# Kernel tuning notes

Measured on AMD Instinct MI355X. Metric: run time of the kernel, lower is better.

Reference implementation:

```python
import jax, jax.numpy as jnp
import numpy as np

B, T, C = 4, 4096, 1024   # batch, seq_len, n_embd
HS = 128                  # tamanho_cabeca (head size)


def setup_inputs() -> dict:
    key = jax.random.key(0)
    kx, kq, kk, kv = jax.random.split(key, 4)
    scale = 0.02
    return {
        "x": jax.random.normal(kx, (B, T, C), dtype=jnp.float32),
        "Wq": jax.random.normal(kq, (C, HS), dtype=jnp.float32) * scale,
        "Wk": jax.random.normal(kk, (C, HS), dtype=jnp.float32) * scale,
        "Wv": jax.random.normal(kv, (C, HS), dtype=jnp.float32) * scale,
    }


def reference(x, Wq, Wk, Wv):
    # Single-head causal self-attention, faithful to the torch Head module.
    _, Tn, Cn = x.shape
    q = jnp.einsum("btc,ch->bth", x, Wq)
    k = jnp.einsum("btc,ch->bth", x, Wk)
    v = jnp.einsum("btc,ch->bth", x, Wv)
    # NOTE: original scales by C**-0.5 (input embed dim), not head_size**-0.5.
    scores = jnp.einsum("bth,bsh->bts", q, k) * (Cn ** -0.5)
    causal = jnp.tril(jnp.ones((Tn, Tn), dtype=bool))  # [T, T]
    scores = jnp.where(causal, scores, -jnp.inf)
    probs = jax.nn.softmax(scores, axis=-1)
    return jnp.einsum("bts,bsh->bth", probs, v)
```

## Files before the change

kernel.cpp:

```cpp
#include <hip/hip_runtime.h>
#include <hip/hip_bf16.h>
#include <math.h>

typedef __attribute__((ext_vector_type(8))) short short8;
typedef __attribute__((ext_vector_type(4))) float f32x4;
typedef unsigned short ushort_t;

#define B_  4
#define T_  4096
#define C_  1024
#define HS_ 128

#define QSCALE 0.04508422002778011f

__device__ const unsigned char NS_[32] = {
    1,1,1,1,2,2,3,3,3,4,4,4,5,5,5,6,6,7,7,7,8,8,8,9,9,9,10,10,11,11,11,11};

__device__ __forceinline__ ushort_t f2bf(float f) {
    unsigned int u = __float_as_uint(f);
    u = (u + 0x7FFFu + ((u >> 16) & 1u)) >> 16;
    return (ushort_t)u;
}
__device__ __forceinline__ ushort_t f2bf_fast(float f) {
    return (ushort_t)((__float_as_uint(f) + 0x8000u) >> 16);
}
__device__ __forceinline__ float bf2f(ushort_t u) {
    return __uint_as_float(((unsigned)u) << 16);
}
__device__ __forceinline__ void async16(const void* g, void* l) {
    __builtin_amdgcn_global_load_lds(
        (const __attribute__((address_space(1))) unsigned int*)g,
        (__attribute__((address_space(3))) unsigned int*)l, 16, 0, 0);
}
__device__ __forceinline__ float exp2fast(float x) {
    return __builtin_amdgcn_exp2f(x);
}
__device__ __forceinline__ f32x4 ldnt4(const float* p) {
    return __builtin_nontemporal_load((const f32x4*)p);
}
__device__ __forceinline__ void stnt8(ushort_t* p, short8 v) {
    __builtin_nontemporal_store(v, (short8*)p);
}

__global__ __launch_bounds__(256) void wt_kernel(
    const float* __restrict__ Wq, const float* __restrict__ Wk,
    const float* __restrict__ Wv, ushort_t* __restrict__ WT3)
{
    __shared__ ushort_t sWT[128 * 68];
    const int blk = blockIdx.x, tid = threadIdx.x;
    const int m = blk >> 4, slab = blk & 15;
    const float* __restrict__ W = (m == 0) ? Wq : (m == 1) ? Wk : Wv;
    const int kc = slab * 64;
    const int r = tid >> 2, h0 = (tid & 3) * 32;
#pragma unroll
    for (int j = 0; j < 8; ++j) {
        float4 wv = *(const float4*)(W + (size_t)(kc + r) * 128 + h0 + j * 4);
        sWT[(h0 + j * 4 + 0) * 68 + r] = f2bf(wv.x);
        sWT[(h0 + j * 4 + 1) * 68 + r] = f2bf(wv.y);
        sWT[(h0 + j * 4 + 2) * 68 + r] = f2bf(wv.z);
        sWT[(h0 + j * 4 + 3) * 68 + r] = f2bf(wv.w);
    }
    __syncthreads();
#pragma unroll
    for (int j = 0; j < 4; ++j) {
        int d = j * 256 + tid;
        int h = d >> 3, c8 = d & 7;
        short8 o;
#pragma unroll
        for (int e = 0; e < 8; ++e) o[e] = (short)sWT[h * 68 + c8 * 8 + e];
        *(short8*)(WT3 + (size_t)(m * 128 + h) * 1024 + kc + c8 * 8) = o;
    }
}

__global__ __launch_bounds__(256, 1) void qkv_gemm(
    const float* __restrict__ x, const ushort_t* __restrict__ WT3,
    ushort_t* __restrict__ q, ushort_t* __restrict__ k,
    ushort_t* __restrict__ vT)
{
    extern __shared__ ushort_t smem[];

    const int tid  = threadIdx.x;
    const int t0   = blockIdx.x * 64;
    const int w    = tid >> 6, lane = tid & 63;
    const int quad = lane >> 4, l15 = lane & 15;

    const int arow = tid >> 3, ac = tid & 7;
    const float* __restrict__ gx = x + (size_t)(t0 + arow) * C_ + ac * 8;
    const int aswz = ((ac ^ (arow & 7)) * 8);

    const ushort_t* gB[12];
    int bdst[12];
#pragma unroll
    for (int j = 0; j < 12; ++j) {
        int d = j * 256 + tid, row = d >> 3, c = d & 7;
        gB[j] = WT3 + (size_t)row * C_ + ((c ^ (row & 7)) * 8);
        bdst[j] = 4096 + d * 8;
    }

    f32x4 acc[4][6];
#pragma unroll
    for (int mt = 0; mt < 4; ++mt)
#pragma unroll
        for (int nt = 0; nt < 6; ++nt) acc[mt][nt] = (f32x4)0.f;

    f32x4 ar[2][2];
#pragma unroll
    for (int p = 0; p < 2; ++p) {
        ar[p][0] = ldnt4(gx + (size_t)(p * 32) * C_);
        ar[p][1] = ldnt4(gx + (size_t)(p * 32) * C_ + 4);
    }
#pragma unroll
    for (int j = 0; j < 12; ++j) async16(gB[j], &smem[bdst[j]]);
#pragma unroll
    for (int p = 0; p < 2; ++p) {
        short8 sv;
        sv[0]=f2bf(ar[p][0][0]); sv[1]=f2bf(ar[p][0][1]);
        sv[2]=f2bf(ar[p][0][2]); sv[3]=f2bf(ar[p][0][3]);
        sv[4]=f2bf(ar[p][1][0]); sv[5]=f2bf(ar[p][1][1]);
        sv[6]=f2bf(ar[p][1][2]); sv[7]=f2bf(ar[p][1][3]);
        *(short8*)&smem[(p * 32 + arow) * 64 + aswz] = sv;
    }
    __syncthreads();

    for (int it = 0; it < 16; ++it) {
        const int buf = it & 1, nb = buf ^ 1;
        const bool more = (it < 15);
        if (more) {
            const int kc = (it + 1) * 64;
#pragma unroll
            for (int p = 0; p < 2; ++p) {
                ar[p][0] = ldnt4(gx + (size_t)(p * 32) * C_ + kc);
                ar[p][1] = ldnt4(gx + (size_t)(p * 32) * C_ + kc + 4);
            }
#pragma unroll
            for (int j = 0; j < 12; ++j)
                async16(gB[j] + kc, &smem[nb * 28672 + bdst[j]]);
        }
        const ushort_t* sA = &smem[buf * 28672];
        const ushort_t* sB = &smem[buf * 28672 + 4096];
#pragma unroll
        for (int kf = 0; kf < 2; ++kf) {
            short8 af[4];
#pragma unroll
            for (int mt = 0; mt < 4; ++mt) {
                int ar_ = mt * 16 + l15;
                af[mt] = *(const short8*)&sA[ar_ * 64 + (((kf * 4 + quad) ^ (ar_ & 7)) * 8)];
            }
#pragma unroll
            for (int nt = 0; nt < 6; ++nt) {
                int row = w * 96 + nt * 16 + l15;
                short8 bf = *(const short8*)&sB[row * 64 + (((kf * 4 + quad) ^ (row & 7)) * 8)];
#pragma unroll
                for (int mt = 0; mt < 4; ++mt)
                    acc[mt][nt] = __builtin_amdgcn_mfma_f32_16x16x32_bf16(af[mt], bf, acc[mt][nt], 0, 0, 0);
            }
        }
        if (more) {
#pragma unroll
            for (int p = 0; p < 2; ++p) {
                short8 sv;
                sv[0]=f2bf(ar[p][0][0]); sv[1]=f2bf(ar[p][0][1]);
                sv[2]=f2bf(ar[p][0][2]); sv[3]=f2bf(ar[p][0][3]);
                sv[4]=f2bf(ar[p][1][0]); sv[5]=f2bf(ar[p][1][1]);
                sv[6]=f2bf(ar[p][1][2]); sv[7]=f2bf(ar[p][1][3]);
                *(short8*)&smem[nb * 28672 + (p * 32 + arow) * 64 + aswz] = sv;
            }
        }
        __syncthreads();
    }

    ushort_t* sE = smem;
    ushort_t* sT = smem + 64 * 264;
#pragma unroll
    for (int nt = 0; nt < 6; ++nt) {
        const int gc = w * 96 + nt * 16;
        if (gc < 256) {
            const float s = (gc < 128) ? QSCALE : 1.0f;
#pragma unroll
            for (int mt = 0; mt < 4; ++mt)
#pragma unroll
                for (int rr = 0; rr < 4; ++rr)
                    sE[(mt * 16 + quad * 4 + rr) * 264 + gc + l15] =
                        f2bf(acc[mt][nt][rr] * s);
        } else {
#pragma unroll
            for (int mt = 0; mt < 4; ++mt)
#pragma unroll
                for (int rr = 0; rr < 4; ++rr)
                    sT[(mt * 16 + quad * 4 + rr) * 132 + (gc - 256) + l15] =
                        f2bf(acc[mt][nt][rr]);
        }
    }
    __syncthreads();
#pragma unroll
    for (int j = 0; j < 4; ++j) {
        int d = j * 256 + tid;
        int row = d >> 4, cs = d & 15;
        *(short8*)(q + (size_t)(t0 + row) * HS_ + cs * 8) =
            *(const short8*)&sE[row * 264 + cs * 8];
    }
#pragma unroll
    for (int j = 0; j < 4; ++j) {
        int d = j * 256 + tid;
        int row = d >> 4, cs = d & 15;
        *(short8*)(k + (size_t)(t0 + row) * HS_ + cs * 8) =
            *(const short8*)&sE[row * 264 + 128 + cs * 8];
    }
    {
        const int bb = t0 >> 12;
        const int tl = t0 & (T_ - 1);
#pragma unroll
        for (int j = 0; j < 4; ++j) {
            int d = j * 256 + tid;
            int h = d >> 3, t8 = d & 7;
            short8 o;
#pragma unroll
            for (int e = 0; e < 8; ++e)
                o[e] = (short)sT[(t8 * 8 + e) * 132 + h];
            *(short8*)(vT + ((size_t)(bb * HS_) + h) * T_ + tl + t8 * 8) = o;
        }
    }
}

__global__ __launch_bounds__(256, 3) void attn_seg(
    const ushort_t* __restrict__ q, const ushort_t* __restrict__ k,
    const ushort_t* __restrict__ vT, ushort_t* __restrict__ Opart,
    float* __restrict__ lseg)
{
    __shared__ ushort_t smem[23552];
    ushort_t* sKb = smem;
    ushort_t* sVb = smem + 8192;
    ushort_t* sP  = smem + 18432;

    const int tid  = threadIdx.x;
    const int bid  = blockIdx.x;
    const int bb   = (bid & 7) >> 1;
    const int seg  = ((bid >> 3) << 1) | (bid & 1);
    const int slot = bb * 192 + seg;
    int r_ = seg;
    int i = 0;
    while (r_ >= NS_[i]) { r_ -= NS_[i]; ++i; }
    const int s    = r_;
    const int ns   = NS_[i];
    const int qb   = i << 7;
    const int nkc  = (i + 1) << 2;
    const int c0   = (nkc * s) / ns;
    const int c1   = (nkc * (s + 1)) / ns;

    const int w    = tid >> 6, lane = tid & 63;
    const int quad = lane >> 4, l15 = lane & 15;
    const size_t bT = (size_t)bb << 12;

    const int kr0 = tid >> 4,          kc0 = tid & 15;
    const int kr1 = (tid + 256) >> 4,  kc1 = (tid + 256) & 15;
    const ushort_t* kp0 = k + (bT + (size_t)c0 * 32 + kr0) * HS_ + ((kc0 ^ (kr0 & 15)) * 8);
    const ushort_t* kp1 = k + (bT + (size_t)c0 * 32 + kr1) * HS_ + ((kc1 ^ (kr1 & 15)) * 8);
    const int vr0 = tid >> 2,          vc0 = tid & 3;
    const int vr1 = (tid + 256) >> 2,  vc1 = (tid + 256) & 3;
    const ushort_t* vp0 = vT + ((size_t)(bb * HS_) + vr0) * T_ + c0 * 32 + vc0 * 8;
    const ushort_t* vp1 = vT + ((size_t)(bb * HS_) + vr1) * T_ + c0 * 32 + vc1 * 8;
    const int vdst0 = vr0 * 40 + vc0 * 8;
    const int vdst1 = vr1 * 40 + vc1 * 8;

    short8 qf[2][4];
#pragma unroll
    for (int mt = 0; mt < 2; ++mt)
#pragma unroll
        for (int kf = 0; kf < 4; ++kf)
            qf[mt][kf] = *(const short8*)(
                q + (bT + qb + w * 32 + mt * 16 + l15) * HS_ + kf * 32 + quad * 8);

    f32x4 O[2][8];
    f32x4 O_l[2];
#pragma unroll
    for (int mt = 0; mt < 2; ++mt) {
        O_l[mt] = (f32x4)0.f;
#pragma unroll
        for (int nt = 0; nt < 8; ++nt) O[mt][nt] = (f32x4)0.f;
    }
    short8 ones;
#pragma unroll
    for (int e = 0; e < 8; ++e) ones[e] = (short)0x3F80;

    {
        short8 v0 = *(const short8*)vp0;
        short8 v1 = *(const short8*)vp1;
        async16(kp0, sKb + tid * 8);
        async16(kp1, sKb + (tid + 256) * 8);
        kp0 += 32 * HS_; kp1 += 32 * HS_; vp0 += 32; vp1 += 32;
        *(short8*)(sVb + vdst0) = v0;
        *(short8*)(sVb + vdst1) = v1;
    }
    __syncthreads();

    for (int c = c0; c < c1; ++c) {
        const int buf = (c - c0) & 1, nb = buf ^ 1;
        const int kb = c << 5;
        const bool more = (c + 1 < c1);
        short8 pv0, pv1;
        if (more) {
            pv0 = *(const short8*)vp0;
            pv1 = *(const short8*)vp1;
            async16(kp0, sKb + nb * 4096 + tid * 8);
            async16(kp1, sKb + nb * 4096 + (tid + 256) * 8);
            kp0 += 32 * HS_; kp1 += 32 * HS_; vp0 += 32; vp1 += 32;
        }
        const ushort_t* sK = sKb + buf * 4096;
        const ushort_t* sV = sVb + buf * 5120;

        f32x4 S[2][2];
        S[0][0] = (f32x4)0.f; S[0][1] = (f32x4)0.f;
        S[1][0] = (f32x4)0.f; S[1][1] = (f32x4)0.f;
#pragma unroll
        for (int nt = 0; nt < 2; ++nt) {
            int row = nt * 16 + l15;
#pragma unroll
            for (int kf = 0; kf < 4; ++kf) {
                short8 bf = *(const short8*)&sK[row * 128 + (((kf * 4 + quad) ^ l15) * 8)];
                S[0][nt] = __builtin_amdgcn_mfma_f32_16x16x32_bf16(qf[0][kf], bf, S[0][nt], 0, 0, 0);
                S[1][nt] = __builtin_amdgcn_mfma_f32_16x16x32_bf16(qf[1][kf], bf, S[1][nt], 0, 0, 0);
            }
        }
        if (kb + 31 > qb + w * 32) {
#pragma unroll
            for (int mt = 0; mt < 2; ++mt)
#pragma unroll
                for (int nt = 0; nt < 2; ++nt)
#pragma unroll
                    for (int rr = 0; rr < 4; ++rr)
                        if (kb + nt * 16 + l15 > qb + w * 32 + mt * 16 + quad * 4 + rr)
                            S[mt][nt][rr] = -1e30f;
        }
#pragma unroll
        for (int mt = 0; mt < 2; ++mt)
#pragma unroll
            for (int nt = 0; nt < 2; ++nt)
#pragma unroll
                for (int rr = 0; rr < 4; ++rr)
                    sP[w * 1280 + (mt * 16 + quad * 4 + rr) * 40 + nt * 16 + l15] =
                        f2bf_fast(exp2fast(S[mt][nt][rr]));
#pragma unroll
        for (int mt = 0; mt < 2; ++mt) {
            short8 pf = *(short8*)&sP[w * 1280 + (mt * 16 + l15) * 40 + quad * 8];
            O_l[mt] = __builtin_amdgcn_mfma_f32_16x16x32_bf16(pf, ones, O_l[mt], 0, 0, 0);
#pragma unroll
            for (int nt = 0; nt < 8; ++nt) {
                short8 vf = *(const short8*)&sV[(nt * 16 + l15) * 40 + quad * 8];
                O[mt][nt] = __builtin_amdgcn_mfma_f32_16x16x32_bf16(pf, vf, O[mt][nt], 0, 0, 0);
            }
        }
        if (more) {
            *(short8*)(sVb + nb * 5120 + vdst0) = pv0;
            *(short8*)(sVb + nb * 5120 + vdst1) = pv1;
        }
        __syncthreads();
    }

    ushort_t* sE = smem;
#pragma unroll
    for (int mt = 0; mt < 2; ++mt)
#pragma unroll
        for (int nt = 0; nt < 8; ++nt)
#pragma unroll
            for (int rr = 0; rr < 4; ++rr)
                sE[(w * 32 + mt * 16 + quad * 4 + rr) * 136 + nt * 16 + l15] =
                    f2bf(O[mt][nt][rr]);
    if (l15 == 0)
#pragma unroll
        for (int mt = 0; mt < 2; ++mt)
#pragma unroll
            for (int rr = 0; rr < 4; ++rr)
                lseg[slot * 128 + w * 32 + mt * 16 + quad * 4 + rr] = O_l[mt][rr];
    __syncthreads();
#pragma unroll
    for (int j = 0; j < 8; ++j) {
        int d = j * 256 + tid;
        int row = d >> 4, cs = d & 15;
        stnt8(Opart + (size_t)slot * 16384 + row * 128 + cs * 8,
              *(const short8*)&sE[row * 136 + cs * 8]);
    }
}

__global__ __launch_bounds__(256) void combine_kernel(
    const ushort_t* __restrict__ Opart, const float* __restrict__ lseg,
    float* __restrict__ out)
{
    const int blk  = blockIdx.x;
    const int tile = blk >> 3, rg = blk & 7;
    const int i    = tile & 31;
    int sb = (tile >> 5) * 192;
    for (int j = 0; j < i; ++j) sb += NS_[j];
    const int ns  = NS_[i];
    const int row = rg * 16 + (threadIdx.x >> 4);
    const int col = (threadIdx.x & 15) * 8;

    const ushort_t* op = Opart + (size_t)sb * 16384 + row * 128 + col;
    const float*    lp = lseg + sb * 128 + row;

    float den = lp[0];
    short8 cur = *(const short8*)op;
    float acc[8];
#pragma unroll
    for (int e = 0; e < 8; ++e) acc[e] = 0.f;
    for (int s = 1; s < ns; ++s) {
        short8 nxt = *(const short8*)(op + (size_t)s * 16384);
        float  dn  = lp[s * 128];
#pragma unroll
        for (int e = 0; e < 8; ++e) acc[e] += bf2f((ushort_t)cur[e]);
        den += dn;
        cur = nxt;
    }
#pragma unroll
    for (int e = 0; e < 8; ++e) acc[e] += bf2f((ushort_t)cur[e]);

    const float inv = 1.0f / den;
    float* o = out + ((size_t)tile * 128 + row) * 128 + col;
    float4 v0 = make_float4(acc[0] * inv, acc[1] * inv, acc[2] * inv, acc[3] * inv);
    float4 v1 = make_float4(acc[4] * inv, acc[5] * inv, acc[6] * inv, acc[7] * inv);
    *(float4*)o = v0;
    *(float4*)(o + 4) = v1;
}

extern "C" void kernel_launch(void* const* d_in, const int* in_sizes, int n_in,
                              void* d_out, int out_size, void* d_ws, size_t ws_size,
                              hipStream_t stream)
{
    const float* x  = (const float*)d_in[0];
    const float* Wq = (const float*)d_in[1];
    const float* Wk = (const float*)d_in[2];
    const float* Wv = (const float*)d_in[3];
    float* out = (float*)d_out;

    ushort_t* WT3 = (ushort_t*)d_ws;
    ushort_t* q   = WT3 + 393216;
    ushort_t* k   = q + 2097152;
    ushort_t* vT  = k + 2097152;
    ushort_t* Opart = vT + 2097152;
    float* lseg   = (float*)(Opart + 768 * 16384);

    wt_kernel<<<48, 256, 0, stream>>>(Wq, Wk, Wv, WT3);
    qkv_gemm<<<256, 256, 114688, stream>>>(x, WT3, q, k, vT);
    attn_seg<<<768, 256, 0, stream>>>(q, k, vT, Opart, lseg);
    combine_kernel<<<1024, 256, 0, stream>>>(Opart, lseg, out);
}
```

Before: 179.1 us.

## Retile QKV GEMM into 128x128 tiles split per projection matrix

The QKV projection GEMM now launches a 128x3 grid. Each block computes a 128-row by 128-column tile for a single projection (q, k or v) instead of a 64-row by 384-column tile covering all three. Shared memory falls to a static 64KB, which allows two blocks per CU, and the warps form a 2x2 grid of 64x64 subtiles. The trade-off is that each x tile is now read and converted to bf16 three times, once per projection, instead of once. The x loads also switch from nontemporal to regular loads.

```diff
diff --git a/kernel.cpp b/kernel.cpp
--- a/kernel.cpp
+++ b/kernel.cpp
@@ -34,9 +34,6 @@
 }
 __device__ __forceinline__ float exp2fast(float x) {
     return __builtin_amdgcn_exp2f(x);
-}
-__device__ __forceinline__ f32x4 ldnt4(const float* p) {
-    return __builtin_nontemporal_load((const f32x4*)p);
 }
 __device__ __forceinline__ void stnt8(ushort_t* p, short8 v) {
     __builtin_nontemporal_store(v, (short8*)p);
@@ -72,53 +69,58 @@
     }
 }
 
-__global__ __launch_bounds__(256, 1) void qkv_gemm(
+__global__ __launch_bounds__(256, 2) void qkv_gemm(
     const float* __restrict__ x, const ushort_t* __restrict__ WT3,
     ushort_t* __restrict__ q, ushort_t* __restrict__ k,
     ushort_t* __restrict__ vT)
 {
-    extern __shared__ ushort_t smem[];
+    __shared__ ushort_t smem[32768];
 
     const int tid  = threadIdx.x;
-    const int t0   = blockIdx.x * 64;
+    const int t0   = blockIdx.x * 128;
+    const int mm   = blockIdx.y;
     const int w    = tid >> 6, lane = tid & 63;
     const int quad = lane >> 4, l15 = lane & 15;
-
-    const int arow = tid >> 3, ac = tid & 7;
-    const float* __restrict__ gx = x + (size_t)(t0 + arow) * C_ + ac * 8;
-    const int aswz = ((ac ^ (arow & 7)) * 8);
-
-    const ushort_t* gB[12];
-    int bdst[12];
-#pragma unroll
-    for (int j = 0; j < 12; ++j) {
+    const int wr   = (w >> 1) * 64;
+    const int wc   = (w & 1) * 64;
+
+    const ushort_t* __restrict__ WTm = WT3 + (size_t)mm * (128 * 1024);
+
+    const float* __restrict__ gxa = x + (size_t)(t0 + (tid >> 3)) * C_ + (tid & 7) * 8;
+    const int aswz = (((tid & 7) ^ ((tid >> 3) & 7)) * 8);
+    const int arow0 = (tid >> 3);
+
+    const ushort_t* gB[4];
+    int bdst[4];
+#pragma unroll
+    for (int j = 0; j < 4; ++j) {
         int d = j * 256 + tid, row = d >> 3, c = d & 7;
-        gB[j] = WT3 + (size_t)row * C_ + ((c ^ (row & 7)) * 8);
-        bdst[j] = 4096 + d * 8;
-    }
-
-    f32x4 acc[4][6];
+        gB[j] = WTm + (size_t)row * C_ + ((c ^ (row & 7)) * 8);
+        bdst[j] = 8192 + d * 8;
+    }
+
+    f32x4 acc[4][4];
 #pragma unroll
     for (int mt = 0; mt < 4; ++mt)
 #pragma unroll
-        for (int nt = 0; nt < 6; ++nt) acc[mt][nt] = (f32x4)0.f;
-
-    f32x4 ar[2][2];
-#pragma unroll
-    for (int p = 0; p < 2; ++p) {
-        ar[p][0] = ldnt4(gx + (size_t)(p * 32) * C_);
-        ar[p][1] = ldnt4(gx + (size_t)(p * 32) * C_ + 4);
-    }
-#pragma unroll
-    for (int j = 0; j < 12; ++j) async16(gB[j], &smem[bdst[j]]);
-#pragma unroll
-    for (int p = 0; p < 2; ++p) {
+        for (int nt = 0; nt < 4; ++nt) acc[mt][nt] = (f32x4)0.f;
+
+    f32x4 ar_[4][2];
+#pragma unroll
+    for (int p = 0; p < 4; ++p) {
+        ar_[p][0] = *(const f32x4*)(gxa + (size_t)(p * 32) * C_);
+        ar_[p][1] = *(const f32x4*)(gxa + (size_t)(p * 32) * C_ + 4);
+    }
+#pragma unroll
+    for (int j = 0; j < 4; ++j) async16(gB[j], &smem[bdst[j]]);
+#pragma unroll
+    for (int p = 0; p < 4; ++p) {
         short8 sv;
-        sv[0]=f2bf(ar[p][0][0]); sv[1]=f2bf(ar[p][0][1]);
-        sv[2]=f2bf(ar[p][0][2]); sv[3]=f2bf(ar[p][0][3]);
-        sv[4]=f2bf(ar[p][1][0]); sv[5]=f2bf(ar[p][1][1]);
-        sv[6]=f2bf(ar[p][1][2]); sv[7]=f2bf(ar[p][1][3]);
-        *(short8*)&smem[(p * 32 + arow) * 64 + aswz] = sv;
+        sv[0]=f2bf(ar_[p][0][0]); sv[1]=f2bf(ar_[p][0][1]);
+        sv[2]=f2bf(ar_[p][0][2]); sv[3]=f2bf(ar_[p][0][3]);
+        sv[4]=f2bf(ar_[p][1][0]); sv[5]=f2bf(ar_[p][1][1]);
+        sv[6]=f2bf(ar_[p][1][2]); sv[7]=f2bf(ar_[p][1][3]);
+        *(short8*)&smem[(p * 32 + arow0) * 64 + aswz] = sv;
     }
     __syncthreads();
 
@@ -128,91 +130,88 @@
         if (more) {
             const int kc = (it + 1) * 64;
 #pragma unroll
-            for (int p = 0; p < 2; ++p) {
-                ar[p][0] = ldnt4(gx + (size_t)(p * 32) * C_ + kc);
-                ar[p][1] = ldnt4(gx + (size_t)(p * 32) * C_ + kc + 4);
-            }
-#pragma unroll
-            for (int j = 0; j < 12; ++j)
-                async16(gB[j] + kc, &smem[nb * 28672 + bdst[j]]);
-        }
-        const ushort_t* sA = &smem[buf * 28672];
-        const ushort_t* sB = &smem[buf * 28672 + 4096];
+            for (int p = 0; p < 4; ++p) {
+                ar_[p][0] = *(const f32x4*)(gxa + (size_t)(p * 32) * C_ + kc);
+                ar_[p][1] = *(const f32x4*)(gxa + (size_t)(p * 32) * C_ + kc + 4);
+            }
+#pragma unroll
+            for (int j = 0; j < 4; ++j)
+                async16(gB[j] + kc, &smem[nb * 16384 + bdst[j]]);
+        }
+        const ushort_t* sA = &smem[buf * 16384];
+        const ushort_t* sB = &smem[buf * 16384 + 8192];
 #pragma unroll
         for (int kf = 0; kf < 2; ++kf) {
-            short8 af[4];
+            const int kc8 = kf * 4 + quad;
+            short8 af[4], bfr[4];
 #pragma unroll
             for (int mt = 0; mt < 4; ++mt) {
-                int ar_ = mt * 16 + l15;
-                af[mt] = *(const short8*)&sA[ar_ * 64 + (((kf * 4 + quad) ^ (ar_ & 7)) * 8)];
-            }
-#pragma unroll
-            for (int nt = 0; nt < 6; ++nt) {
-                int row = w * 96 + nt * 16 + l15;
-                short8 bf = *(const short8*)&sB[row * 64 + (((kf * 4 + quad) ^ (row & 7)) * 8)];
-#pragma unroll
-                for (int mt = 0; mt < 4; ++mt)
-                    acc[mt][nt] = __builtin_amdgcn_mfma_f32_16x16x32_bf16(af[mt], bf, acc[mt][nt], 0, 0, 0);
-            }
+                int r = wr + mt * 16 + l15;
+                af[mt] = *(const short8*)&sA[r * 64 + ((kc8 ^ (r & 7)) * 8)];
+            }
+#pragma unroll
+            for (int nt = 0; nt < 4; ++nt) {
+                int r = wc + nt * 16 + l15;
+                bfr[nt] = *(const short8*)&sB[r * 64 + ((kc8 ^ (r & 7)) * 8)];
+            }
+#pragma unroll
+            for (int mt = 0; mt < 4; ++mt)
+#pragma unroll
+                for (int nt = 0; nt < 4; ++nt)
+                    acc[mt][nt] = __builtin_amdgcn_mfma_f32_16x16x32_bf16(
+                        af[mt], bfr[nt], acc[mt][nt], 0, 0, 0);
         }
         if (more) {
 #pragma unroll
-            for (int p = 0; p < 2; ++p) {
+            for (int p = 0; p < 4; ++p) {
                 short8 sv;
-                sv[0]=f2bf(ar[p][0][0]); sv[1]=f2bf(ar[p][0][1]);
-                sv[2]=f2bf(ar[p][0][2]); sv[3]=f2bf(ar[p][0][3]);
-                sv[4]=f2bf(ar[p][1][0]); sv[5]=f2bf(ar[p][1][1]);
-                sv[6]=f2bf(ar[p][1][2]); sv[7]=f2bf(ar[p][1][3]);
-                *(short8*)&smem[nb * 28672 + (p * 32 + arow) * 64 + aswz] = sv;
+                sv[0]=f2bf(ar_[p][0][0]); sv[1]=f2bf(ar_[p][0][1]);
+                sv[2]=f2bf(ar_[p][0][2]); sv[3]=f2bf(ar_[p][0][3]);
+                sv[4]=f2bf(ar_[p][1][0]); sv[5]=f2bf(ar_[p][1][1]);
+                sv[6]=f2bf(ar_[p][1][2]); sv[7]=f2bf(ar_[p][1][3]);
+                *(short8*)&smem[nb * 16384 + (p * 32 + arow0) * 64 + aswz] = sv;
             }
         }
         __syncthreads();
     }
 
-    ushort_t* sE = smem;
-    ushort_t* sT = smem + 64 * 264;
-#pragma unroll
-    for (int nt = 0; nt < 6; ++nt) {
-        const int gc = w * 96 + nt * 16;
-        if (gc < 256) {
-            const float s = (gc < 128) ? QSCALE : 1.0f;
-#pragma unroll
-            for (int mt = 0; mt < 4; ++mt)
+    if (mm < 2) {
+        ushort_t* __restrict__ outp = (mm == 0) ? q : k;
+        const float s = (mm == 0) ? QSCALE : 1.0f;
+        ushort_t* sE = smem;
+#pragma unroll
+        for (int mt = 0; mt < 4; ++mt)
+#pragma unroll
+            for (int nt = 0; nt < 4; ++nt)
 #pragma unroll
                 for (int rr = 0; rr < 4; ++rr)
-                    sE[(mt * 16 + quad * 4 + rr) * 264 + gc + l15] =
+                    sE[(wr + mt * 16 + quad * 4 + rr) * 136 + wc + nt * 16 + l15] =
                         f2bf(acc[mt][nt][rr] * s);
-        } else {
-#pragma unroll
-            for (int mt = 0; mt < 4; ++mt)
+        __syncthreads();
+#pragma unroll
+        for (int j = 0; j < 8; ++j) {
+            int d = j * 256 + tid;
+            int row = d >> 4, cs = d & 15;
+            *(short8*)(outp + (size_t)(t0 + row) * HS_ + cs * 8) =
+                *(const short8*)&sE[row * 136 + cs * 8];
+        }
+    } else {
+        ushort_t* sT = smem;
+#pragma unroll
+        for (int mt = 0; mt < 4; ++mt)
+#pragma unroll
+            for (int nt = 0; nt < 4; ++nt)
 #pragma unroll
                 for (int rr = 0; rr < 4; ++rr)
-                    sT[(mt * 16 + quad * 4 + rr) * 132 + (gc - 256) + l15] =
+                    sT[(wr + mt * 16 + quad * 4 + rr) * 132 + wc + nt * 16 + l15] =
                         f2bf(acc[mt][nt][rr]);
-        }
-    }
-    __syncthreads();
-#pragma unroll
-    for (int j = 0; j < 4; ++j) {
-        int d = j * 256 + tid;
-        int row = d >> 4, cs = d & 15;
-        *(short8*)(q + (size_t)(t0 + row) * HS_ + cs * 8) =
-            *(const short8*)&sE[row * 264 + cs * 8];
-    }
-#pragma unroll
-    for (int j = 0; j < 4; ++j) {
-        int d = j * 256 + tid;
-        int row = d >> 4, cs = d & 15;
-        *(short8*)(k + (size_t)(t0 + row) * HS_ + cs * 8) =
-            *(const short8*)&sE[row * 264 + 128 + cs * 8];
-    }
-    {
+        __syncthreads();
         const int bb = t0 >> 12;
         const int tl = t0 & (T_ - 1);
 #pragma unroll
-        for (int j = 0; j < 4; ++j) {
+        for (int j = 0; j < 8; ++j) {
             int d = j * 256 + tid;
-            int h = d >> 3, t8 = d & 7;
+            int h = d >> 4, t8 = d & 15;
             short8 o;
 #pragma unroll
             for (int e = 0; e < 8; ++e)
@@ -439,7 +438,7 @@
     float* lseg   = (float*)(Opart + 768 * 16384);
 
     wt_kernel<<<48, 256, 0, stream>>>(Wq, Wk, Wv, WT3);
-    qkv_gemm<<<256, 256, 114688, stream>>>(x, WT3, q, k, vT);
+    qkv_gemm<<<dim3(128, 3), 256, 0, stream>>>(x, WT3, q, k, vT);
     attn_seg<<<768, 256, 0, stream>>>(q, k, vT, Opart, lseg);
     combine_kernel<<<1024, 256, 0, stream>>>(Opart, lseg, out);
 }
```

Measured after the change: 172.6 us. 1.04x faster.
